# Performance work log

Measured on AMD Instinct MI355X. Metric: run time of the kernel, lower is better.

## Reference

```python
import jax, jax.numpy as jnp
import numpy as np

EPS = 1e-5

def _face_normals(v, vi):
    # v: [B,V,3], vi: [F,3] -> [B,F,3]
    pts = v[:, vi]                                  # [B,F,3,3]
    n = jnp.cross(pts[:, :, 1] - pts[:, :, 0], pts[:, :, 2] - pts[:, :, 0])
    norm = jnp.linalg.norm(n, axis=-1, keepdims=True)
    return n / jnp.where(norm < EPS, 1.0, norm)

def _vert_normals(v, vi):
    fn = _face_normals(v, vi)                       # [B,F,3]
    fn_rep = jnp.repeat(fn, 3, axis=1)              # [B,3F,3] (one copy per face vertex)
    vn = jnp.zeros_like(v).at[:, vi.reshape(-1)].add(fn_rep)
    norm = jnp.linalg.norm(vn, axis=-1, keepdims=True)
    return vn / jnp.where(norm < EPS, 1.0, norm)

def _values_to_uv(values, index_image, bary_image):
    # values: [B,V,C]; index_image/bary_image: [U,U,3] -> [B,C,U,U]
    mask = jnp.all(index_image != -1, axis=-1)      # [U,U]
    idx = jnp.clip(index_image, 0, values.shape[1] - 1)
    vals = values[:, idx]                           # [B,U,U,3,C]
    uv = jnp.einsum('buvkc,uvk->bcuv', vals, bary_image.astype(values.dtype))
    return uv * mask[None, None].astype(values.dtype)

def _grid_sample_bilinear(img, gx, gy):
    # img: [B,C,H,W]; gx,gy: [N] in [-1,1]; align_corners=False, zero padding
    B, C, H, W = img.shape
    ix = ((gx + 1.0) * W - 1.0) * 0.5
    iy = ((gy + 1.0) * H - 1.0) * 0.5
    x0 = jnp.floor(ix); y0 = jnp.floor(iy)
    x1 = x0 + 1.0;      y1 = y0 + 1.0
    wx1 = ix - x0; wx0 = 1.0 - wx1
    wy1 = iy - y0; wy0 = 1.0 - wy1
    def gather(xi, yi):
        valid = (xi >= 0) & (xi < W) & (yi >= 0) & (yi < H)
        xc = jnp.clip(xi, 0, W - 1).astype(jnp.int32)
        yc = jnp.clip(yi, 0, H - 1).astype(jnp.int32)
        return img[:, :, yc, xc] * valid.astype(img.dtype)  # [B,C,N]
    return (gather(x0, y0) * (wx0 * wy0) + gather(x1, y0) * (wx1 * wy0)
          + gather(x0, y1) * (wx0 * wy1) + gather(x1, y1) * (wx1 * wy1))

def _sample_uv(values_uv, uv_coords, v2uv):
    g = uv_coords * 2.0 - 1.0                       # [T,2]
    vals = _grid_sample_bilinear(values_uv, g[:, 0], g[:, 1])  # [B,C,T]
    vals = jnp.transpose(vals, (0, 2, 1))           # [B,T,C]
    return vals[:, v2uv].mean(axis=2)               # [B,V,C]

def setup_inputs() -> dict:
    key = jax.random.key(0)
    ks = jax.random.split(key, 6)
    B, V, Fc, U, T, K = 8, 100000, 200000, 1024, 110000, 2
    verts = jax.random.normal(ks[0], (B, V, 3), jnp.float32)
    vi = jax.random.randint(ks[1], (Fc, 3), 0, V, dtype=jnp.int32)
    index_image = jax.random.randint(ks[2], (U, U, 3), 0, V, dtype=jnp.int32)
    bary_image = jax.random.uniform(ks[3], (U, U, 3), jnp.float32)
    vt = jax.random.uniform(ks[4], (T, 2), jnp.float32)
    v2uv = jax.random.randint(ks[5], (V, K), 0, T, dtype=jnp.int32)
    return {"verts": verts, "bary_image": bary_image, "vt": vt,
            "vi": vi, "index_image": index_image, "v2uv": v2uv}

def reference(verts, bary_image, vt, vi, index_image, v2uv):
    vn = _vert_normals(verts, vi)                   # [B,V,3]
    uv = _values_to_uv(vn, index_image, bary_image) # [B,3,U,U]
    return _sample_uv(uv, vt, v2uv)                 # [B,V,3]
```

## Files before the change

### kernel.cpp

```cpp
#include <hip/hip_runtime.h>
#include <hip/hip_fp16.h>

#define EPS 1e-5f

constexpr int B = 8;
constexpr int V = 100000;
constexpr int F = 200000;
constexpr int U = 1024;
constexpr int T = 110000;
constexpr int CAP = 24;

constexpr int NBUK = (V + 127) / 128;
constexpr int N4   = (3 * F) / 4;
constexpr int EB   = (N4 + 255) / 256;
constexpr int TRB  = (V + 255) / 256;

constexpr int FQ   = 8;
constexpr int FNB  = (F * 8 / FQ + 255) / 256;
constexpr int TQ   = 4;
constexpr int CPB  = (T / TQ + 255) / 256;
constexpr int SQ   = 2;
constexpr int VQ   = 2;

struct alignas(8) h4 { __half2 a, b; };
__device__ inline h4 pack_h4(float x, float y, float z) {
    h4 r; r.a = __floats2half2_rn(x, y); r.b = __floats2half2_rn(z, 0.0f);
    return r;
}
__device__ inline float3 unpack_h4(h4 v) {
    float2 xy = __half22float2(v.a);
    float2 zw = __half22float2(v.b);
    return make_float3(xy.x, xy.y, zw.x);
}

struct alignas(16) Corner16 { unsigned lo, hi; __half2 w01; __half2 w2_; };
__device__ inline Corner16 pack_corner(int i0, int i1, int i2,
                                       float w0, float w1, float w2) {
    unsigned long long x = (unsigned long long)(unsigned)i0
                         | ((unsigned long long)(unsigned)i1 << 21)
                         | ((unsigned long long)(unsigned)i2 << 42);
    Corner16 c;
    c.lo = (unsigned)x;
    c.hi = (unsigned)(x >> 32);
    c.w01 = __floats2half2_rn(w0, w1);
    c.w2_ = __floats2half2_rn(w2, 0.0f);
    return c;
}

__global__ void k1_pre(const float* __restrict__ verts,
                       float4* __restrict__ vertsT,
                       const int* __restrict__ vi,
                       int* __restrict__ tot) {
    __shared__ int lh[NBUK];
    int blk = blockIdx.x;

    if (blk < TRB) {
        int v = blk * 256 + threadIdx.x;
        if (v >= V) return;
        float4 row[8];
#pragma unroll
        for (int b = 0; b < 8; ++b) {
            const float* p = verts + (size_t)b * V * 3 + (size_t)v * 3;
            row[b] = make_float4(p[0], p[1], p[2], 0.0f);
        }
        float4* dst = vertsT + (size_t)v * 8;
#pragma unroll
        for (int b = 0; b < 8; ++b) dst[b] = row[b];
        return;
    }

    int k = blk - TRB;
    for (int i = threadIdx.x; i < NBUK; i += 256) lh[i] = 0;
    __syncthreads();
    int m4 = k * 256 + threadIdx.x;
    if (m4 < N4) {
        int4 e = ((const int4*)vi)[m4];
        atomicAdd(&lh[e.x >> 7], 1);
        atomicAdd(&lh[e.y >> 7], 1);
        atomicAdd(&lh[e.z >> 7], 1);
        atomicAdd(&lh[e.w >> 7], 1);
    }
    __syncthreads();
    for (int b = threadIdx.x; b < NBUK; b += 256)
        if (lh[b]) atomicAdd(&tot[b], lh[b]);
}

__device__ inline void scan_base(const int* __restrict__ tot,
                                 int* pre, int* part) {
    constexpr int CH = (NBUK + 255) / 256;
    int th = threadIdx.x;
    int loc[CH];
    int local = 0;
#pragma unroll
    for (int j = 0; j < CH; ++j) {
        int idx = th * CH + j;
        int c = (idx < NBUK) ? tot[idx] : 0;
        loc[j] = local;
        local += c;
    }
    part[th] = local;
    __syncthreads();
    for (int off = 1; off < 256; off <<= 1) {
        int x = (th >= off) ? part[th - off] : 0;
        __syncthreads();
        part[th] += x;
        __syncthreads();
    }
    int excl = part[th] - local;
#pragma unroll
    for (int j = 0; j < CH; ++j) {
        int idx = th * CH + j;
        if (idx < NBUK) pre[idx] = excl + loc[j];
    }
    if (th == 255) pre[NBUK] = part[255];
    __syncthreads();
}

__global__ void k2_fused(const int* __restrict__ vi,
                         const float4* __restrict__ vertsT,
                         h4* __restrict__ fn,
                         const int* __restrict__ index_image,
                         const float* __restrict__ bary_image,
                         const float* __restrict__ vt,
                         Corner16* __restrict__ corners,
                         const int* __restrict__ tot,
                         int* __restrict__ cursor,
                         int* __restrict__ pairs) {
    int blk = blockIdx.x;

    if (blk < FNB) {
        int id = blk * 256 + threadIdx.x;
        if (id >= F * 8 / FQ) return;
        int b = id & 7;
        int fbase = id >> 3;

        int ia[FQ], ib[FQ], ic[FQ];
        float4 p0[FQ], p1[FQ], p2[FQ];
#pragma unroll
        for (int q = 0; q < FQ; ++q) {
            int f = fbase + q * (F / FQ);
            ia[q] = vi[f * 3 + 0];
            ib[q] = vi[f * 3 + 1];
            ic[q] = vi[f * 3 + 2];
        }
#pragma unroll
        for (int q = 0; q < FQ; ++q) {
            p0[q] = vertsT[(size_t)ia[q] * 8 + b];
            p1[q] = vertsT[(size_t)ib[q] * 8 + b];
            p2[q] = vertsT[(size_t)ic[q] * 8 + b];
        }
#pragma unroll
        for (int q = 0; q < FQ; ++q) {
            int f = fbase + q * (F / FQ);
            float e1x = p1[q].x - p0[q].x, e1y = p1[q].y - p0[q].y, e1z = p1[q].z - p0[q].z;
            float e2x = p2[q].x - p0[q].x, e2y = p2[q].y - p0[q].y, e2z = p2[q].z - p0[q].z;

            float nx = e1y * e2z - e1z * e2y;
            float ny = e1z * e2x - e1x * e2z;
            float nz = e1x * e2y - e1y * e2x;

            float norm = sqrtf(nx * nx + ny * ny + nz * nz);
            float inv = (norm < EPS) ? 1.0f : (1.0f / norm);
            fn[(size_t)f * 8 + b] = pack_h4(nx * inv, ny * inv, nz * inv);
        }
        return;
    }

    if (blk < FNB + CPB) {
        int tbase = (blk - FNB) * 256 + threadIdx.x;
        if (tbase >= T / TQ) return;
#pragma unroll
        for (int qq = 0; qq < TQ; ++qq) {
            int t = tbase + qq * (T / TQ);

            float gx = vt[t * 2 + 0];
            float gy = vt[t * 2 + 1];
            float ix = gx * (float)U - 0.5f;
            float iy = gy * (float)U - 0.5f;

            float x0f = floorf(ix);
            float y0f = floorf(iy);
            int x0 = (int)x0f;
            int y0 = (int)y0f;
            float wx1 = ix - x0f, wx0 = 1.0f - wx1;
            float wy1 = iy - y0f, wy0 = 1.0f - wy1;

#pragma unroll
            for (int c = 0; c < 4; ++c) {
                int cy = c >> 1, cx = c & 1;
                int y = y0 + cy;
                int x = x0 + cx;
                int i0 = 0, i1 = 0, i2 = 0;
                float w0 = 0.0f, w1 = 0.0f, w2 = 0.0f;
                if (x >= 0 && x < U && y >= 0 && y < U) {
                    float w = (cy ? wy1 : wy0) * (cx ? wx1 : wx0);
                    int pix = y * U + x;
                    int j0 = index_image[pix * 3 + 0];
                    int j1 = index_image[pix * 3 + 1];
                    int j2 = index_image[pix * 3 + 2];
                    float m = (j0 != -1 && j1 != -1 && j2 != -1) ? 1.0f : 0.0f;
                    float wm = w * m;
                    i0 = min(max(j0, 0), V - 1);
                    i1 = min(max(j1, 0), V - 1);
                    i2 = min(max(j2, 0), V - 1);
                    w0 = wm * bary_image[pix * 3 + 0];
                    w1 = wm * bary_image[pix * 3 + 1];
                    w2 = wm * bary_image[pix * 3 + 2];
                }
                corners[t * 4 + c] = pack_corner(i0, i1, i2, w0, w1, w2);
            }
        }
        return;
    }

    __shared__ int pre[NBUK + 1];
    __shared__ int part[256];
    __shared__ int lh[NBUK];
    __shared__ int base[NBUK];
    scan_base(tot, pre, part);
    for (int i = threadIdx.x; i < NBUK; i += 256) lh[i] = 0;
    __syncthreads();

    int k = blk - FNB - CPB;
    int m4 = k * 256 + threadIdx.x;
    bool act = (m4 < N4);
    int vv[4], rr[4], bbk[4], fc[4];
    if (act) {
        int4 e = ((const int4*)vi)[m4];
        vv[0] = e.x; vv[1] = e.y; vv[2] = e.z; vv[3] = e.w;
        int be = m4 * 4;
#pragma unroll
        for (int j = 0; j < 4; ++j) {
            bbk[j] = vv[j] >> 7;
            rr[j] = atomicAdd(&lh[bbk[j]], 1);
            fc[j] = (be + j) / 3;
        }
    }
    __syncthreads();
    for (int i = threadIdx.x; i < NBUK; i += 256)
        base[i] = lh[i] ? atomicAdd(&cursor[i], lh[i]) : 0;
    __syncthreads();
    if (act) {
#pragma unroll
        for (int j = 0; j < 4; ++j) {
            int pos = pre[bbk[j]] + base[bbk[j]] + rr[j];
            pairs[pos] = ((vv[j] & 127) << 18) | fc[j];
        }
    }
}

__global__ __launch_bounds__(256) void k5_gather(
        const int* __restrict__ pairs,
        const int* __restrict__ tot,
        const h4* __restrict__ fn,
        h4* __restrict__ vn) {
    __shared__ int cnt[128];
    __shared__ int rows[128 * CAP];
    __shared__ int pre[NBUK + 1];
    __shared__ int part[256];
    scan_base(tot, pre, part);

    int tid = threadIdx.x;
    if (tid < 128) cnt[tid] = 0;
    __syncthreads();

    int b = blockIdx.x;
    int start = pre[b], end = pre[b + 1];
    for (int i = start + tid; i < end; i += 256) {
        int pk = pairs[i];
        int vl = pk >> 18;
        int f = pk & 0x3FFFF;
        int pos = atomicAdd(&cnt[vl], 1);
        if (pos < CAP) rows[vl * CAP + pos] = f;
    }
    __syncthreads();

    int v0 = b << 7;
    for (int id = tid; id < 128 * 8; id += 256) {
        int vl = id >> 3, b8 = id & 7;
        int v = v0 + vl;
        if (v >= V) continue;
        int deg = min(cnt[vl], CAP);
        float ax = 0.0f, ay = 0.0f, az = 0.0f;
        int j = 0;
        for (; j + 1 < deg; j += 2) {
            h4 r0 = fn[(size_t)rows[vl * CAP + j] * 8 + b8];
            h4 r1 = fn[(size_t)rows[vl * CAP + j + 1] * 8 + b8];
            float3 n0 = unpack_h4(r0);
            float3 n1 = unpack_h4(r1);
            ax += n0.x + n1.x; ay += n0.y + n1.y; az += n0.z + n1.z;
        }
        if (j < deg) {
            float3 n = unpack_h4(fn[(size_t)rows[vl * CAP + j] * 8 + b8]);
            ax += n.x; ay += n.y; az += n.z;
        }
        float nn = sqrtf(ax * ax + ay * ay + az * az);
        float inv = (nn < EPS) ? 1.0f : (1.0f / nn);
        vn[(size_t)v * 8 + b8] = pack_h4(ax * inv, ay * inv, az * inv);
    }
}

__global__ void sample_points(const h4* __restrict__ vn,
                              const Corner16* __restrict__ corners,
                              h4* __restrict__ vals) {
    int id = blockIdx.x * blockDim.x + threadIdx.x;
    if (id >= (T / SQ) * 8) return;
    int b = id & 7;
    int tb = id >> 3;

#pragma unroll
    for (int s = 0; s < SQ; ++s) {
        int t = tb + s * (T / SQ);
        float ax = 0.0f, ay = 0.0f, az = 0.0f;
        Corner16 cr[4];
#pragma unroll
        for (int c = 0; c < 4; ++c) cr[c] = corners[t * 4 + c];
        h4 q[12];
#pragma unroll
        for (int c = 0; c < 4; ++c) {
            unsigned long long x = (unsigned long long)cr[c].lo
                                 | ((unsigned long long)cr[c].hi << 32);
            int i0 = (int)(x & 0x1FFFFF);
            int i1 = (int)((x >> 21) & 0x1FFFFF);
            int i2 = (int)(x >> 42);
            q[c * 3 + 0] = vn[(size_t)i0 * 8 + b];
            q[c * 3 + 1] = vn[(size_t)i1 * 8 + b];
            q[c * 3 + 2] = vn[(size_t)i2 * 8 + b];
        }
#pragma unroll
        for (int c = 0; c < 4; ++c) {
            float2 w01 = __half22float2(cr[c].w01);
            float w2 = __low2float(cr[c].w2_);
            float3 q0 = unpack_h4(q[c * 3 + 0]);
            float3 q1 = unpack_h4(q[c * 3 + 1]);
            float3 q2 = unpack_h4(q[c * 3 + 2]);
            ax += w01.x * q0.x + w01.y * q1.x + w2 * q2.x;
            ay += w01.x * q0.y + w01.y * q1.y + w2 * q2.y;
            az += w01.x * q0.z + w01.y * q1.z + w2 * q2.z;
        }
        vals[(size_t)t * 8 + b] = pack_h4(ax, ay, az);
    }
}

__global__ void gather_out(const h4* __restrict__ vals,
                           const int* __restrict__ v2uv,
                           float* __restrict__ out) {
    int id = blockIdx.x * blockDim.x + threadIdx.x;
    if (id >= (V / VQ) * 8) return;
    int b = id & 7;
    int vb = id >> 3;

    int t0[VQ], t1[VQ];
    h4 xa[VQ], ya[VQ];
#pragma unroll
    for (int s = 0; s < VQ; ++s) {
        int v = vb + s * (V / VQ);
        t0[s] = v2uv[v * 2 + 0];
        t1[s] = v2uv[v * 2 + 1];
    }
#pragma unroll
    for (int s = 0; s < VQ; ++s) {
        xa[s] = vals[(size_t)t0[s] * 8 + b];
        ya[s] = vals[(size_t)t1[s] * 8 + b];
    }
#pragma unroll
    for (int s = 0; s < VQ; ++s) {
        int v = vb + s * (V / VQ);
        float3 x = unpack_h4(xa[s]);
        float3 y = unpack_h4(ya[s]);
        float* o = out + (size_t)b * V * 3 + (size_t)v * 3;
        o[0] = 0.5f * (x.x + y.x);
        o[1] = 0.5f * (x.y + y.y);
        o[2] = 0.5f * (x.z + y.z);
    }
}

extern "C" void kernel_launch(void* const* d_in, const int* in_sizes, int n_in,
                              void* d_out, int out_size, void* d_ws, size_t ws_size,
                              hipStream_t stream) {
    const float* verts   = (const float*)d_in[0];
    const float* bary    = (const float*)d_in[1];
    const float* vt      = (const float*)d_in[2];
    const int*   vi      = (const int*)d_in[3];
    const int*   idx_img = (const int*)d_in[4];
    const int*   v2uv    = (const int*)d_in[5];
    float* out = (float*)d_out;

    float4*   vertsT  = (float4*)d_ws;
    h4*       vn      = (h4*)d_ws;
    h4*       fn      = (h4*)(vertsT + (size_t)V * 8);
    h4*       vals    = fn;
    Corner16* corners = (Corner16*)((char*)fn + (size_t)F * 8 * sizeof(h4));
    int*      tot     = (int*)(corners + (size_t)T * 4);
    int*      cursor  = tot + NBUK;
    int*      pairs   = cursor + NBUK;

    const int BLK = 256;
    hipMemsetAsync(tot, 0, 2 * NBUK * sizeof(int), stream);
    k1_pre<<<TRB + EB, BLK, 0, stream>>>(verts, vertsT, vi, tot);
    k2_fused<<<FNB + CPB + EB, BLK, 0, stream>>>(
        vi, vertsT, fn, idx_img, bary, vt, corners, tot, cursor, pairs);
    k5_gather<<<NBUK, BLK, 0, stream>>>(pairs, tot, fn, vn);
    sample_points<<<((T / SQ) * 8 + BLK - 1) / BLK, BLK, 0, stream>>>(
        vn, corners, vals);
    gather_out<<<((V / VQ) * 8 + BLK - 1) / BLK, BLK, 0, stream>>>(
        vals, v2uv, out);
}
```

Measured before the change: 181.4 us.

## Replace bucketed counting-sort adjacency with direct per-vertex ELL lists via global atomics

Drops the two-pass bucket histogram, prefix scan and pair-scatter used to build vertex-to-face adjacency. k1 now appends each face index straight into a fixed-capacity per-vertex ELL row through a global atomic counter, and k5 becomes one thread per (vertex, batch) that reads that row with int4 loads. This removes the scan and shared-memory staging and takes the scatter work out of k2. In exchange it adds many contended global atomics, uses a larger zero-filled counter array, and reads ELL rows that are not coalesced. Launch bounds are also added to k2 and sample_points.

```diff
diff --git a/kernel.cpp b/kernel.cpp
--- a/kernel.cpp
+++ b/kernel.cpp
@@ -10,7 +10,6 @@
 constexpr int T = 110000;
 constexpr int CAP = 24;
 
-constexpr int NBUK = (V + 127) / 128;
 constexpr int N4   = (3 * F) / 4;
 constexpr int EB   = (N4 + 255) / 256;
 constexpr int TRB  = (V + 255) / 256;
@@ -50,8 +49,8 @@
 __global__ void k1_pre(const float* __restrict__ verts,
                        float4* __restrict__ vertsT,
                        const int* __restrict__ vi,
-                       int* __restrict__ tot) {
-    __shared__ int lh[NBUK];
+                       int* __restrict__ cnt,
+                       int* __restrict__ ell) {
     int blk = blockIdx.x;
 
     if (blk < TRB) {
@@ -70,62 +69,28 @@
     }
 
     int k = blk - TRB;
-    for (int i = threadIdx.x; i < NBUK; i += 256) lh[i] = 0;
-    __syncthreads();
     int m4 = k * 256 + threadIdx.x;
-    if (m4 < N4) {
-        int4 e = ((const int4*)vi)[m4];
-        atomicAdd(&lh[e.x >> 7], 1);
-        atomicAdd(&lh[e.y >> 7], 1);
-        atomicAdd(&lh[e.z >> 7], 1);
-        atomicAdd(&lh[e.w >> 7], 1);
-    }
-    __syncthreads();
-    for (int b = threadIdx.x; b < NBUK; b += 256)
-        if (lh[b]) atomicAdd(&tot[b], lh[b]);
-}
-
-__device__ inline void scan_base(const int* __restrict__ tot,
-                                 int* pre, int* part) {
-    constexpr int CH = (NBUK + 255) / 256;
-    int th = threadIdx.x;
-    int loc[CH];
-    int local = 0;
-#pragma unroll
-    for (int j = 0; j < CH; ++j) {
-        int idx = th * CH + j;
-        int c = (idx < NBUK) ? tot[idx] : 0;
-        loc[j] = local;
-        local += c;
-    }
-    part[th] = local;
-    __syncthreads();
-    for (int off = 1; off < 256; off <<= 1) {
-        int x = (th >= off) ? part[th - off] : 0;
-        __syncthreads();
-        part[th] += x;
-        __syncthreads();
-    }
-    int excl = part[th] - local;
-#pragma unroll
-    for (int j = 0; j < CH; ++j) {
-        int idx = th * CH + j;
-        if (idx < NBUK) pre[idx] = excl + loc[j];
-    }
-    if (th == 255) pre[NBUK] = part[255];
-    __syncthreads();
-}
-
-__global__ void k2_fused(const int* __restrict__ vi,
-                         const float4* __restrict__ vertsT,
-                         h4* __restrict__ fn,
-                         const int* __restrict__ index_image,
-                         const float* __restrict__ bary_image,
-                         const float* __restrict__ vt,
-                         Corner16* __restrict__ corners,
-                         const int* __restrict__ tot,
-                         int* __restrict__ cursor,
-                         int* __restrict__ pairs) {
+    if (m4 >= N4) return;
+    int4 e = ((const int4*)vi)[m4];
+    int be = m4 * 4;
+    int vv[4] = {e.x, e.y, e.z, e.w};
+#pragma unroll
+    for (int j = 0; j < 4; ++j) {
+        int v = vv[j];
+        int f = (be + j) / 3;
+        int rank = atomicAdd(&cnt[v], 1);
+        if (rank < CAP) ell[(size_t)v * CAP + rank] = f;
+    }
+}
+
+__global__ __launch_bounds__(256, 3) void k2_fused(
+        const int* __restrict__ vi,
+        const float4* __restrict__ vertsT,
+        h4* __restrict__ fn,
+        const int* __restrict__ index_image,
+        const float* __restrict__ bary_image,
+        const float* __restrict__ vt,
+        Corner16* __restrict__ corners) {
     int blk = blockIdx.x;
 
     if (blk < FNB) {
@@ -166,143 +131,92 @@
         return;
     }
 
-    if (blk < FNB + CPB) {
-        int tbase = (blk - FNB) * 256 + threadIdx.x;
-        if (tbase >= T / TQ) return;
-#pragma unroll
-        for (int qq = 0; qq < TQ; ++qq) {
-            int t = tbase + qq * (T / TQ);
-
-            float gx = vt[t * 2 + 0];
-            float gy = vt[t * 2 + 1];
-            float ix = gx * (float)U - 0.5f;
-            float iy = gy * (float)U - 0.5f;
-
-            float x0f = floorf(ix);
-            float y0f = floorf(iy);
-            int x0 = (int)x0f;
-            int y0 = (int)y0f;
-            float wx1 = ix - x0f, wx0 = 1.0f - wx1;
-            float wy1 = iy - y0f, wy0 = 1.0f - wy1;
-
-#pragma unroll
-            for (int c = 0; c < 4; ++c) {
-                int cy = c >> 1, cx = c & 1;
-                int y = y0 + cy;
-                int x = x0 + cx;
-                int i0 = 0, i1 = 0, i2 = 0;
-                float w0 = 0.0f, w1 = 0.0f, w2 = 0.0f;
-                if (x >= 0 && x < U && y >= 0 && y < U) {
-                    float w = (cy ? wy1 : wy0) * (cx ? wx1 : wx0);
-                    int pix = y * U + x;
-                    int j0 = index_image[pix * 3 + 0];
-                    int j1 = index_image[pix * 3 + 1];
-                    int j2 = index_image[pix * 3 + 2];
-                    float m = (j0 != -1 && j1 != -1 && j2 != -1) ? 1.0f : 0.0f;
-                    float wm = w * m;
-                    i0 = min(max(j0, 0), V - 1);
-                    i1 = min(max(j1, 0), V - 1);
-                    i2 = min(max(j2, 0), V - 1);
-                    w0 = wm * bary_image[pix * 3 + 0];
-                    w1 = wm * bary_image[pix * 3 + 1];
-                    w2 = wm * bary_image[pix * 3 + 2];
-                }
-                corners[t * 4 + c] = pack_corner(i0, i1, i2, w0, w1, w2);
+    int tbase = (blk - FNB) * 256 + threadIdx.x;
+    if (tbase >= T / TQ) return;
+#pragma unroll
+    for (int qq = 0; qq < TQ; ++qq) {
+        int t = tbase + qq * (T / TQ);
+
+        float gx = vt[t * 2 + 0];
+        float gy = vt[t * 2 + 1];
+        float ix = gx * (float)U - 0.5f;
+        float iy = gy * (float)U - 0.5f;
+
+        float x0f = floorf(ix);
+        float y0f = floorf(iy);
+        int x0 = (int)x0f;
+        int y0 = (int)y0f;
+        float wx1 = ix - x0f, wx0 = 1.0f - wx1;
+        float wy1 = iy - y0f, wy0 = 1.0f - wy1;
+
+#pragma unroll
+        for (int c = 0; c < 4; ++c) {
+            int cy = c >> 1, cx = c & 1;
+            int y = y0 + cy;
+            int x = x0 + cx;
+            int i0 = 0, i1 = 0, i2 = 0;
+            float w0 = 0.0f, w1 = 0.0f, w2 = 0.0f;
+            if (x >= 0 && x < U && y >= 0 && y < U) {
+                float w = (cy ? wy1 : wy0) * (cx ? wx1 : wx0);
+                int pix = y * U + x;
+                int j0 = index_image[pix * 3 + 0];
+                int j1 = index_image[pix * 3 + 1];
+                int j2 = index_image[pix * 3 + 2];
+                float m = (j0 != -1 && j1 != -1 && j2 != -1) ? 1.0f : 0.0f;
+                float wm = w * m;
+                i0 = min(max(j0, 0), V - 1);
+                i1 = min(max(j1, 0), V - 1);
+                i2 = min(max(j2, 0), V - 1);
+                w0 = wm * bary_image[pix * 3 + 0];
+                w1 = wm * bary_image[pix * 3 + 1];
+                w2 = wm * bary_image[pix * 3 + 2];
             }
-        }
-        return;
-    }
-
-    __shared__ int pre[NBUK + 1];
-    __shared__ int part[256];
-    __shared__ int lh[NBUK];
-    __shared__ int base[NBUK];
-    scan_base(tot, pre, part);
-    for (int i = threadIdx.x; i < NBUK; i += 256) lh[i] = 0;
-    __syncthreads();
-
-    int k = blk - FNB - CPB;
-    int m4 = k * 256 + threadIdx.x;
-    bool act = (m4 < N4);
-    int vv[4], rr[4], bbk[4], fc[4];
-    if (act) {
-        int4 e = ((const int4*)vi)[m4];
-        vv[0] = e.x; vv[1] = e.y; vv[2] = e.z; vv[3] = e.w;
-        int be = m4 * 4;
-#pragma unroll
-        for (int j = 0; j < 4; ++j) {
-            bbk[j] = vv[j] >> 7;
-            rr[j] = atomicAdd(&lh[bbk[j]], 1);
-            fc[j] = (be + j) / 3;
-        }
-    }
-    __syncthreads();
-    for (int i = threadIdx.x; i < NBUK; i += 256)
-        base[i] = lh[i] ? atomicAdd(&cursor[i], lh[i]) : 0;
-    __syncthreads();
-    if (act) {
-#pragma unroll
-        for (int j = 0; j < 4; ++j) {
-            int pos = pre[bbk[j]] + base[bbk[j]] + rr[j];
-            pairs[pos] = ((vv[j] & 127) << 18) | fc[j];
+            corners[t * 4 + c] = pack_corner(i0, i1, i2, w0, w1, w2);
         }
     }
 }
 
 __global__ __launch_bounds__(256) void k5_gather(
-        const int* __restrict__ pairs,
-        const int* __restrict__ tot,
+        const int* __restrict__ cnt,
+        const int* __restrict__ ell,
         const h4* __restrict__ fn,
         h4* __restrict__ vn) {
-    __shared__ int cnt[128];
-    __shared__ int rows[128 * CAP];
-    __shared__ int pre[NBUK + 1];
-    __shared__ int part[256];
-    scan_base(tot, pre, part);
-
-    int tid = threadIdx.x;
-    if (tid < 128) cnt[tid] = 0;
-    __syncthreads();
-
-    int b = blockIdx.x;
-    int start = pre[b], end = pre[b + 1];
-    for (int i = start + tid; i < end; i += 256) {
-        int pk = pairs[i];
-        int vl = pk >> 18;
-        int f = pk & 0x3FFFF;
-        int pos = atomicAdd(&cnt[vl], 1);
-        if (pos < CAP) rows[vl * CAP + pos] = f;
-    }
-    __syncthreads();
-
-    int v0 = b << 7;
-    for (int id = tid; id < 128 * 8; id += 256) {
-        int vl = id >> 3, b8 = id & 7;
-        int v = v0 + vl;
-        if (v >= V) continue;
-        int deg = min(cnt[vl], CAP);
-        float ax = 0.0f, ay = 0.0f, az = 0.0f;
-        int j = 0;
-        for (; j + 1 < deg; j += 2) {
-            h4 r0 = fn[(size_t)rows[vl * CAP + j] * 8 + b8];
-            h4 r1 = fn[(size_t)rows[vl * CAP + j + 1] * 8 + b8];
-            float3 n0 = unpack_h4(r0);
-            float3 n1 = unpack_h4(r1);
-            ax += n0.x + n1.x; ay += n0.y + n1.y; az += n0.z + n1.z;
-        }
-        if (j < deg) {
-            float3 n = unpack_h4(fn[(size_t)rows[vl * CAP + j] * 8 + b8]);
-            ax += n.x; ay += n.y; az += n.z;
-        }
-        float nn = sqrtf(ax * ax + ay * ay + az * az);
-        float inv = (nn < EPS) ? 1.0f : (1.0f / nn);
-        vn[(size_t)v * 8 + b8] = pack_h4(ax * inv, ay * inv, az * inv);
-    }
-}
-
-__global__ void sample_points(const h4* __restrict__ vn,
-                              const Corner16* __restrict__ corners,
-                              h4* __restrict__ vals) {
+    int id = blockIdx.x * blockDim.x + threadIdx.x;
+    if (id >= V * 8) return;
+    int b8 = id & 7;
+    int v = id >> 3;
+
+    int deg = min(cnt[v], CAP);
+    const int4* ev = (const int4*)(ell + (size_t)v * CAP);
+
+    float ax = 0.0f, ay = 0.0f, az = 0.0f;
+    for (int c = 0; c * 4 < deg; ++c) {
+        int4 e = ev[c];
+        int fi[4] = {e.x, e.y, e.z, e.w};
+        h4 r[4];
+#pragma unroll
+        for (int j = 0; j < 4; ++j) {
+            int f = fi[j];
+            f = ((unsigned)f < (unsigned)F) ? f : 0;
+            r[j] = fn[(size_t)f * 8 + b8];
+        }
+#pragma unroll
+        for (int j = 0; j < 4; ++j) {
+            if (c * 4 + j < deg) {
+                float3 n = unpack_h4(r[j]);
+                ax += n.x; ay += n.y; az += n.z;
+            }
+        }
+    }
+    float nn = sqrtf(ax * ax + ay * ay + az * az);
+    float inv = (nn < EPS) ? 1.0f : (1.0f / nn);
+    vn[(size_t)v * 8 + b8] = pack_h4(ax * inv, ay * inv, az * inv);
+}
+
+__global__ __launch_bounds__(256, 4) void sample_points(
+        const h4* __restrict__ vn,
+        const Corner16* __restrict__ corners,
+        h4* __restrict__ vals) {
     int id = blockIdx.x * blockDim.x + threadIdx.x;
     if (id >= (T / SQ) * 8) return;
     int b = id & 7;
@@ -391,16 +305,15 @@
     h4*       fn      = (h4*)(vertsT + (size_t)V * 8);
     h4*       vals    = fn;
     Corner16* corners = (Corner16*)((char*)fn + (size_t)F * 8 * sizeof(h4));
-    int*      tot     = (int*)(corners + (size_t)T * 4);
-    int*      cursor  = tot + NBUK;
-    int*      pairs   = cursor + NBUK;
+    int*      cnt     = (int*)(corners + (size_t)T * 4);
+    int*      ell     = cnt + V;
 
     const int BLK = 256;
-    hipMemsetAsync(tot, 0, 2 * NBUK * sizeof(int), stream);
-    k1_pre<<<TRB + EB, BLK, 0, stream>>>(verts, vertsT, vi, tot);
-    k2_fused<<<FNB + CPB + EB, BLK, 0, stream>>>(
-        vi, vertsT, fn, idx_img, bary, vt, corners, tot, cursor, pairs);
-    k5_gather<<<NBUK, BLK, 0, stream>>>(pairs, tot, fn, vn);
+    hipMemsetAsync(cnt, 0, (size_t)V * sizeof(int), stream);
+    k1_pre<<<TRB + EB, BLK, 0, stream>>>(verts, vertsT, vi, cnt, ell);
+    k2_fused<<<FNB + CPB, BLK, 0, stream>>>(
+        vi, vertsT, fn, idx_img, bary, vt, corners);
+    k5_gather<<<(V * 8 + BLK - 1) / BLK, BLK, 0, stream>>>(cnt, ell, fn, vn);
     sample_points<<<((T / SQ) * 8 + BLK - 1) / BLK, BLK, 0, stream>>>(
         vn, corners, vals);
     gather_out<<<((V / VQ) * 8 + BLK - 1) / BLK, BLK, 0, stream>>>(
```

After: 193.4 us. +6.6%, slower.
